# Kernel tuning notes

Measured on AMD Instinct MI355X. Metric: run time of the kernel, lower is better.

The kernel has to match this reference:

```python
import jax, jax.numpy as jnp
import numpy as np

B, C_IN, H, W = 64, 2, 64, 64   # batch, input channels, grid
HID, ACT, ITERS, K = 150, 8, 20, 64  # conv_h channels, actions, VI iters, num query states


def _conv(x, w, pad):
    # NCHW conv, stride 1, symmetric padding
    return jax.lax.conv_general_dilated(
        x, w, window_strides=(1, 1), padding=[(pad, pad), (pad, pad)],
        dimension_numbers=("NCHW", "OIHW", "NCHW"))


def setup_inputs() -> dict:
    key = jax.random.key(0)
    ks = jax.random.split(key, 7)
    X = jax.random.normal(ks[0], (B, C_IN, H, W), jnp.float32)
    S1 = jax.random.randint(ks[1], (K,), 0, H)
    S2 = jax.random.randint(ks[2], (K,), 0, W)
    Wh = jax.random.normal(ks[3], (HID, C_IN, 3, 3), jnp.float32) * 0.1
    bh = jax.random.normal(ks[4], (HID,), jnp.float32) * 0.1
    Wr = jax.random.normal(ks[5], (1, HID, 1, 1), jnp.float32) * 0.1
    Wq = jax.random.normal(ks[6], (ACT, 2, 3, 3), jnp.float32) * 0.1
    return {"X": X, "S1": S1, "S2": S2, "Wh": Wh, "bh": bh, "Wr": Wr, "Wq": Wq}


def reference(X, S1, S2, Wh, bh, Wr, Wq):
    h = _conv(X, Wh, 1) + bh[None, :, None, None]   # [B,150,H,W]
    r = _conv(h, Wr, 0)                              # [B,1,H,W] reward map
    v0 = jnp.zeros_like(r)
    q0 = jnp.zeros((B, ACT, H, W), r.dtype)

    def body(carry, _):
        v, _q = carry
        rv = jnp.concatenate([r, v], axis=1)         # [B,2,H,W]
        q = _conv(rv, Wq, 1)                         # [B,8,H,W]
        v = jnp.max(q, axis=1, keepdims=True)        # [B,1,H,W]
        return (v, q), None

    (v, q), _ = jax.lax.scan(body, (v0, q0), None, length=ITERS)
    # q[:, :, S1, S2][0] then transpose -> [K, ACT]
    q_out = q[0][:, S1, S2].T
    return jax.nn.softmax(q_out, axis=1)
```

## Files before the change

### kernel.cpp

```cpp
#include <hip/hip_runtime.h>


#define ACT 8
#define HID 150
#define STR 76

typedef float v2f __attribute__((ext_vector_type(2)));
typedef unsigned long long u64;

__device__ __forceinline__ void pkfma_lo(v2f& acc, u64 wp, v2f x) {
  asm("v_pk_fma_f32 %0, %1, %2, %0 op_sel:[0,0,0] op_sel_hi:[0,1,1]"
      : "+v"(acc) : "s"(wp), "v"(x));
}
__device__ __forceinline__ void pkfma_hi(v2f& acc, u64 wp, v2f x) {
  asm("v_pk_fma_f32 %0, %1, %2, %0 op_sel:[1,0,0] op_sel_hi:[1,1,1]"
      : "+v"(acc) : "s"(wp), "v"(x));
}
__device__ __forceinline__ void pkfma_s(v2f& acc, u64 wp, int half, v2f x) {
  if (half == 0) pkfma_lo(acc, wp, x); else pkfma_hi(acc, wp, x);
}
__device__ __forceinline__ v2f cmax(v2f a, v2f b) {
  return (v2f){fmaxf(a.x, b.x), fmaxf(a.y, b.y)};
}
__device__ __forceinline__ v2f cfma(float w, v2f x, v2f acc) {
  acc.x = fmaf(w, x.x, acc.x);
  acc.y = fmaf(w, x.y, acc.y);
  return acc;
}
__device__ __forceinline__ float uload(const float* p) {
  return __int_as_float(__builtin_amdgcn_readfirstlane(__float_as_int(*p)));
}
__device__ __forceinline__ float lane_prev(float x) {
  return __int_as_float(
      __builtin_amdgcn_update_dpp(0, __float_as_int(x), 0x138, 0xF, 0xF, true));
}
__device__ __forceinline__ float lane_next(float x) {
  return __int_as_float(
      __builtin_amdgcn_update_dpp(0, __float_as_int(x), 0x130, 0xF, 0xF, true));
}

__launch_bounds__(1024, 4)
__global__ void vin_kernel(const float* __restrict__ X,
                           const int*   __restrict__ S1,
                           const int*   __restrict__ S2,
                           const float* __restrict__ Wh,
                           const float* __restrict__ bh,
                           const float* __restrict__ Wr,
                           const float* __restrict__ Wq,
                           float*       __restrict__ out) {
  __shared__ float r_s[66][STR];
  __shared__ float v_s[66][STR];
  __shared__ v2f   tb[2][34][32];
  __shared__ v2f   bb[2][34][32];
  __shared__ float weff_s[19];
  __shared__ int   s12_s[128];

  const int tid  = threadIdx.x;
  const int tx   = tid & 31;
  const int ty   = tid >> 5;
  const int lane = tid & 63;
  const float zp = (lane == 32) ? 0.f : 1.f;
  const float zn = (lane == 31) ? 0.f : 1.f;
  const int R  = ty << 1;
  const int cc = tx << 1;

  {
    const float4 z = make_float4(0.f, 0.f, 0.f, 0.f);
    float4* a = (float4*)&r_s[0][0];
    for (int i = tid; i < 66 * STR / 4; i += 1024) a[i] = z;
    float4* b = (float4*)&v_s[0][0];
    for (int i = tid; i < 66 * STR / 4; i += 1024) b[i] = z;
    float4* c = (float4*)&tb[0][0][0];
    for (int i = tid; i < 2 * 34 * 32 / 2; i += 1024) c[i] = z;
    float4* d = (float4*)&bb[0][0][0];
    for (int i = tid; i < 2 * 34 * 32 / 2; i += 1024) d[i] = z;
  }
  if (tid < 128) s12_s[tid] = (tid < 64) ? S1[tid] : S2[tid - 64];

  if (tid < 19 * 32) {
    const int t = tid >> 5, ln = tid & 31;
    float acc = 0.f;
    #pragma unroll
    for (int i = 0; i < 5; ++i) {
      const int h = ln + 32 * i;
      if (h < HID) acc += Wr[h] * (t < 18 ? Wh[h * 18 + t] : bh[h]);
    }
    acc += __shfl_xor(acc, 1);
    acc += __shfl_xor(acc, 2);
    acc += __shfl_xor(acc, 4);
    acc += __shfl_xor(acc, 8);
    acc += __shfl_xor(acc, 16);
    if (ln == 0) weff_s[t] = acc;
  }
  __syncthreads();

  v2f ra, rb;
  {
    v2f xx[2][4];
    #pragma unroll
    for (int ch = 0; ch < 2; ++ch)
      #pragma unroll
      for (int dy = 0; dy < 4; ++dy) {
        const int row = R - 1 + dy;
        xx[ch][dy] = (row >= 0 && row < 64)
                   ? *(const v2f*)&X[ch * 4096 + row * 64 + cc]
                   : (v2f){0.f, 0.f};
      }
    float wl[18];
    #pragma unroll
    for (int t = 0; t < 18; ++t) wl[t] = uload(&weff_s[t]);
    const float beff = uload(&weff_s[18]);
    v2f a0 = (v2f){beff, beff}, a1 = a0;
    #pragma unroll
    for (int ch = 0; ch < 2; ++ch) {
      v2f L[4], Rr[4];
      #pragma unroll
      for (int i = 0; i < 4; ++i) {
        L[i]  = (v2f){lane_prev(xx[ch][i].y) * zp, xx[ch][i].x};
        Rr[i] = (v2f){xx[ch][i].y, lane_next(xx[ch][i].x) * zn};
      }
      #pragma unroll
      for (int dy = 0; dy < 3; ++dy) {
        const float w0 = wl[ch * 9 + dy * 3 + 0];
        const float w1 = wl[ch * 9 + dy * 3 + 1];
        const float w2 = wl[ch * 9 + dy * 3 + 2];
        a0 = cfma(w0, L[dy], a0);     a0 = cfma(w1, xx[ch][dy], a0);
        a0 = cfma(w2, Rr[dy], a0);
        a1 = cfma(w0, L[dy + 1], a1); a1 = cfma(w1, xx[ch][dy + 1], a1);
        a1 = cfma(w2, Rr[dy + 1], a1);
      }
    }
    *(v2f*)&r_s[R + 1][cc + 4] = a0;
    *(v2f*)&r_s[R + 2][cc + 4] = a1;
    ra = a0; rb = a1;
  }
  __syncthreads();

  v2f qr0[ACT], qr1[ACT], v0, v1;
  {
    v2f rows[4];
    rows[0] = *(const v2f*)&r_s[R][cc + 4];
    rows[1] = ra;
    rows[2] = rb;
    rows[3] = *(const v2f*)&r_s[R + 3][cc + 4];
    v2f L[4], Rr[4];
    #pragma unroll
    for (int i = 0; i < 4; ++i) {
      L[i]  = (v2f){lane_prev(rows[i].y) * zp, rows[i].x};
      Rr[i] = (v2f){rows[i].y, lane_next(rows[i].x) * zn};
    }
    #pragma unroll
    for (int a = 0; a < ACT; ++a) {
      v2f q0 = (v2f){0.f, 0.f}, q1 = (v2f){0.f, 0.f};
      #pragma unroll
      for (int dy = 0; dy < 3; ++dy) {
        const float w0 = uload(&Wq[a * 18 + dy * 3 + 0]);
        const float w1 = uload(&Wq[a * 18 + dy * 3 + 1]);
        const float w2 = uload(&Wq[a * 18 + dy * 3 + 2]);
        q0 = cfma(w0, L[dy], q0);     q0 = cfma(w1, rows[dy], q0);
        q0 = cfma(w2, Rr[dy], q0);
        q1 = cfma(w0, L[dy + 1], q1); q1 = cfma(w1, rows[dy + 1], q1);
        q1 = cfma(w2, Rr[dy + 1], q1);
      }
      qr0[a] = q0; qr1[a] = q1;
      v0 = a ? cmax(v0, q0) : q0;
      v1 = a ? cmax(v1, q1) : q1;
    }
    tb[0][ty + 1][tx] = v0;
    bb[0][ty + 1][tx] = v1;
  }

  u64 wqp[36];
  #pragma unroll
  for (int p = 0; p < 36; ++p) {
    const int w0 = 2 * p, w1 = 2 * p + 1;
    const unsigned lo = (unsigned)__builtin_amdgcn_readfirstlane(
        __float_as_int(Wq[(w0 / 9) * 18 + 9 + (w0 % 9)]));
    const unsigned hi = (unsigned)__builtin_amdgcn_readfirstlane(
        __float_as_int(Wq[(w1 / 9) * 18 + 9 + (w1 % 9)]));
    wqp[p] = (u64)lo | ((u64)hi << 32);
  }
  __syncthreads();

  #pragma unroll 1
  for (int it = 0; it < 9; ++it) {
    #pragma unroll
    for (int p = 0; p < 2; ++p) {
      v2f rows[4];
      rows[0] = bb[p][ty][tx];
      rows[1] = v0;
      rows[2] = v1;
      rows[3] = tb[p][ty + 2][tx];
      v2f L[4], Rr[4];
      #pragma unroll
      for (int i = 0; i < 4; ++i) {
        L[i]  = (v2f){lane_prev(rows[i].y) * zp, rows[i].x};
        Rr[i] = (v2f){rows[i].y, lane_next(rows[i].x) * zn};
      }
      v2f m0, m1;
      #pragma unroll
      for (int a = 0; a < ACT; ++a) {
        v2f q0 = qr0[a], q1 = qr1[a];
        #pragma unroll
        for (int dy = 0; dy < 3; ++dy) {
          const int w0 = a * 9 + dy * 3 + 0;
          const int w1 = a * 9 + dy * 3 + 1;
          const int w2 = a * 9 + dy * 3 + 2;
          pkfma_s(q0, wqp[w0 >> 1], w0 & 1, L[dy]);
          pkfma_s(q0, wqp[w1 >> 1], w1 & 1, rows[dy]);
          pkfma_s(q0, wqp[w2 >> 1], w2 & 1, Rr[dy]);
          pkfma_s(q1, wqp[w0 >> 1], w0 & 1, L[dy + 1]);
          pkfma_s(q1, wqp[w1 >> 1], w1 & 1, rows[dy + 1]);
          pkfma_s(q1, wqp[w2 >> 1], w2 & 1, Rr[dy + 1]);
        }
        m0 = a ? cmax(m0, q0) : q0;
        m1 = a ? cmax(m1, q1) : q1;
      }
      v0 = m0; v1 = m1;
      tb[p ^ 1][ty + 1][tx] = v0;
      bb[p ^ 1][ty + 1][tx] = v1;
      __syncthreads();
    }
  }

  *(v2f*)&v_s[R + 1][cc + 4] = v0;
  *(v2f*)&v_s[R + 2][cc + 4] = v1;
  __syncthreads();

  if (tid < 64 * ACT) {
    const int k = tid >> 3;
    const int a = tid & 7;
    const int qy = s12_s[k];
    const int qx = s12_s[64 + k];
    float accq = 0.f;
    #pragma unroll
    for (int dy = 0; dy < 3; ++dy)
      #pragma unroll
      for (int dx = 0; dx < 3; ++dx) {
        const float w0 = Wq[a * 18 + dy * 3 + dx];
        const float w1 = Wq[a * 18 + 9 + dy * 3 + dx];
        accq += w0 * r_s[qy + dy][qx + dx + 3];
        accq += w1 * v_s[qy + dy][qx + dx + 3];
      }
    float m = accq;
    m = fmaxf(m, __shfl_xor(m, 1));
    m = fmaxf(m, __shfl_xor(m, 2));
    m = fmaxf(m, __shfl_xor(m, 4));
    const float e = __expf(accq - m);
    float s = e;
    s += __shfl_xor(s, 1);
    s += __shfl_xor(s, 2);
    s += __shfl_xor(s, 4);
    out[tid] = e / s;
  }
}

extern "C" void kernel_launch(void* const* d_in, const int* in_sizes, int n_in,
                              void* d_out, int out_size, void* d_ws, size_t ws_size,
                              hipStream_t stream) {
  const float* X  = (const float*)d_in[0];
  const int*   S1 = (const int*)d_in[1];
  const int*   S2 = (const int*)d_in[2];
  const float* Wh = (const float*)d_in[3];
  const float* bh = (const float*)d_in[4];
  const float* Wr = (const float*)d_in[5];
  const float* Wq = (const float*)d_in[6];
  float* out = (float*)d_out;

  vin_kernel<<<1, 1024, 0, stream>>>(X, S1, S2, Wh, bh, Wr, Wq, out);
}
```

Measured before the change: 96.88 us.

## Split grid across two workgroups with overlapping halo and shrinking active region

Splits the 64-row grid into two 52-row overlapping slabs, each handled by its own 832-thread workgroup, so the value-iteration stencil runs on two compute units instead of one. The halo (extra rows) lets each block iterate independently without inter-block sync; rows whose results become invalid are masked off progressively each step. The cost is redundant computation in the overlap region, and each block still only writes outputs for query states in its half.

```diff
diff --git a/kernel.cpp b/kernel.cpp
--- a/kernel.cpp
+++ b/kernel.cpp
@@ -4,6 +4,8 @@
 #define ACT 8
 #define HID 150
 #define STR 76
+#define NB   26
+#define NTHR (NB * 32)
 
 typedef float v2f __attribute__((ext_vector_type(2)));
 typedef unsigned long long u64;
@@ -39,7 +41,7 @@
       __builtin_amdgcn_update_dpp(0, __float_as_int(x), 0x130, 0xF, 0xF, true));
 }
 
-__launch_bounds__(1024, 4)
+__launch_bounds__(NTHR, 4)
 __global__ void vin_kernel(const float* __restrict__ X,
                            const int*   __restrict__ S1,
                            const int*   __restrict__ S2,
@@ -48,10 +50,10 @@
                            const float* __restrict__ Wr,
                            const float* __restrict__ Wq,
                            float*       __restrict__ out) {
-  __shared__ float r_s[66][STR];
-  __shared__ float v_s[66][STR];
-  __shared__ v2f   tb[2][34][32];
-  __shared__ v2f   bb[2][34][32];
+  __shared__ float r_s[54][STR];
+  __shared__ float v_s[54][STR];
+  __shared__ v2f   tb[2][28][32];
+  __shared__ v2f   bb[2][28][32];
   __shared__ float weff_s[19];
   __shared__ int   s12_s[128];
 
@@ -61,19 +63,21 @@
   const int lane = tid & 63;
   const float zp = (lane == 32) ? 0.f : 1.f;
   const float zn = (lane == 31) ? 0.f : 1.f;
-  const int R  = ty << 1;
+  const int Rl = ty << 1;
   const int cc = tx << 1;
+  const int wg = blockIdx.x;
+  const int B  = wg * 12;
 
   {
     const float4 z = make_float4(0.f, 0.f, 0.f, 0.f);
     float4* a = (float4*)&r_s[0][0];
-    for (int i = tid; i < 66 * STR / 4; i += 1024) a[i] = z;
+    for (int i = tid; i < 54 * STR / 4; i += NTHR) a[i] = z;
     float4* b = (float4*)&v_s[0][0];
-    for (int i = tid; i < 66 * STR / 4; i += 1024) b[i] = z;
+    for (int i = tid; i < 54 * STR / 4; i += NTHR) b[i] = z;
     float4* c = (float4*)&tb[0][0][0];
-    for (int i = tid; i < 2 * 34 * 32 / 2; i += 1024) c[i] = z;
+    for (int i = tid; i < 2 * 28 * 32 / 2; i += NTHR) c[i] = z;
     float4* d = (float4*)&bb[0][0][0];
-    for (int i = tid; i < 2 * 34 * 32 / 2; i += 1024) d[i] = z;
+    for (int i = tid; i < 2 * 28 * 32 / 2; i += NTHR) d[i] = z;
   }
   if (tid < 128) s12_s[tid] = (tid < 64) ? S1[tid] : S2[tid - 64];
 
@@ -101,9 +105,9 @@
     for (int ch = 0; ch < 2; ++ch)
       #pragma unroll
       for (int dy = 0; dy < 4; ++dy) {
-        const int row = R - 1 + dy;
-        xx[ch][dy] = (row >= 0 && row < 64)
-                   ? *(const v2f*)&X[ch * 4096 + row * 64 + cc]
+        const int g = B + Rl - 1 + dy;
+        xx[ch][dy] = (g >= 0 && g < 64)
+                   ? *(const v2f*)&X[ch * 4096 + g * 64 + cc]
                    : (v2f){0.f, 0.f};
       }
     float wl[18];
@@ -130,8 +134,8 @@
         a1 = cfma(w2, Rr[dy + 1], a1);
       }
     }
-    *(v2f*)&r_s[R + 1][cc + 4] = a0;
-    *(v2f*)&r_s[R + 2][cc + 4] = a1;
+    *(v2f*)&r_s[Rl + 1][cc + 4] = a0;
+    *(v2f*)&r_s[Rl + 2][cc + 4] = a1;
     ra = a0; rb = a1;
   }
   __syncthreads();
@@ -139,10 +143,10 @@
   v2f qr0[ACT], qr1[ACT], v0, v1;
   {
     v2f rows[4];
-    rows[0] = *(const v2f*)&r_s[R][cc + 4];
+    rows[0] = *(const v2f*)&r_s[Rl][cc + 4];
     rows[1] = ra;
     rows[2] = rb;
-    rows[3] = *(const v2f*)&r_s[R + 3][cc + 4];
+    rows[3] = *(const v2f*)&r_s[Rl + 3][cc + 4];
     v2f L[4], Rr[4];
     #pragma unroll
     for (int i = 0; i < 4; ++i) {
@@ -182,10 +186,9 @@
   }
   __syncthreads();
 
-  #pragma unroll 1
-  for (int it = 0; it < 9; ++it) {
-    #pragma unroll
-    for (int p = 0; p < 2; ++p) {
+  auto vi = [&](int s, int p) {
+    const bool act = (wg == 0) ? (Rl <= 49 - s) : (Rl >= s + 1);
+    if (act) {
       v2f rows[4];
       rows[0] = bb[p][ty][tx];
       rows[1] = v0;
@@ -203,15 +206,15 @@
         v2f q0 = qr0[a], q1 = qr1[a];
         #pragma unroll
         for (int dy = 0; dy < 3; ++dy) {
-          const int w0 = a * 9 + dy * 3 + 0;
-          const int w1 = a * 9 + dy * 3 + 1;
-          const int w2 = a * 9 + dy * 3 + 2;
-          pkfma_s(q0, wqp[w0 >> 1], w0 & 1, L[dy]);
-          pkfma_s(q0, wqp[w1 >> 1], w1 & 1, rows[dy]);
-          pkfma_s(q0, wqp[w2 >> 1], w2 & 1, Rr[dy]);
-          pkfma_s(q1, wqp[w0 >> 1], w0 & 1, L[dy + 1]);
-          pkfma_s(q1, wqp[w1 >> 1], w1 & 1, rows[dy + 1]);
-          pkfma_s(q1, wqp[w2 >> 1], w2 & 1, Rr[dy + 1]);
+          const int i0 = a * 9 + dy * 3 + 0;
+          const int i1 = a * 9 + dy * 3 + 1;
+          const int i2 = a * 9 + dy * 3 + 2;
+          pkfma_s(q0, wqp[i0 >> 1], i0 & 1, L[dy]);
+          pkfma_s(q0, wqp[i1 >> 1], i1 & 1, rows[dy]);
+          pkfma_s(q0, wqp[i2 >> 1], i2 & 1, Rr[dy]);
+          pkfma_s(q1, wqp[i0 >> 1], i0 & 1, L[dy + 1]);
+          pkfma_s(q1, wqp[i1 >> 1], i1 & 1, rows[dy + 1]);
+          pkfma_s(q1, wqp[i2 >> 1], i2 & 1, Rr[dy + 1]);
         }
         m0 = a ? cmax(m0, q0) : q0;
         m1 = a ? cmax(m1, q1) : q1;
@@ -219,12 +222,17 @@
       v0 = m0; v1 = m1;
       tb[p ^ 1][ty + 1][tx] = v0;
       bb[p ^ 1][ty + 1][tx] = v1;
-      __syncthreads();
-    }
-  }
-
-  *(v2f*)&v_s[R + 1][cc + 4] = v0;
-  *(v2f*)&v_s[R + 2][cc + 4] = v1;
+    }
+    __syncthreads();
+  };
+  #pragma unroll 1
+  for (int it = 0; it < 9; ++it) {
+    vi(2 * it, 0);
+    vi(2 * it + 1, 1);
+  }
+
+  *(v2f*)&v_s[Rl + 1][cc + 4] = v0;
+  *(v2f*)&v_s[Rl + 2][cc + 4] = v1;
   __syncthreads();
 
   if (tid < 64 * ACT) {
@@ -232,6 +240,8 @@
     const int a = tid & 7;
     const int qy = s12_s[k];
     const int qx = s12_s[64 + k];
+    const bool mine = (wg == 0) ? (qy <= 31) : (qy >= 32);
+    const int ly = mine ? (qy - B) : 25;
     float accq = 0.f;
     #pragma unroll
     for (int dy = 0; dy < 3; ++dy)
@@ -239,8 +249,8 @@
       for (int dx = 0; dx < 3; ++dx) {
         const float w0 = Wq[a * 18 + dy * 3 + dx];
         const float w1 = Wq[a * 18 + 9 + dy * 3 + dx];
-        accq += w0 * r_s[qy + dy][qx + dx + 3];
-        accq += w1 * v_s[qy + dy][qx + dx + 3];
+        accq += w0 * r_s[ly + dy][qx + dx + 3];
+        accq += w1 * v_s[ly + dy][qx + dx + 3];
       }
     float m = accq;
     m = fmaxf(m, __shfl_xor(m, 1));
@@ -251,7 +261,7 @@
     s += __shfl_xor(s, 1);
     s += __shfl_xor(s, 2);
     s += __shfl_xor(s, 4);
-    out[tid] = e / s;
+    if (mine) out[tid] = e / s;
   }
 }
 
@@ -267,5 +277,5 @@
   const float* Wq = (const float*)d_in[6];
   float* out = (float*)d_out;
 
-  vin_kernel<<<1, 1024, 0, stream>>>(X, S1, S2, Wh, bh, Wr, Wq, out);
-}
+  vin_kernel<<<2, NTHR, 0, stream>>>(X, S1, S2, Wh, bh, Wr, Wq, out);
+}
```

New measurement: 91.58 us. -5.5%, faster.
